# Kernel optimization log

Measured on AMD Instinct MI355X. Metric: run time of the kernel, lower is better.

## Reference

```python
import jax, jax.numpy as jnp
import numpy as np

B, NN, HL = 64, 64, 50
IN_DIM, POS_DIM, ATT_DIM = 384, 64, 256
NEWS_DIM = IN_DIM + POS_DIM  # 448


def setup_inputs() -> dict:
    key = jax.random.key(0)
    ks = jax.random.split(key, 8)
    pos_emb = jax.random.uniform(ks[3], (100, POS_DIM), jnp.float32, -0.1, 0.1)
    pos_emb = pos_emb.at[0].set(0.0)  # initialize() zeros row 0
    return {
        "log_vec": jax.random.normal(ks[0], (B, HL, IN_DIM), jnp.float32),
        "log_mask": jax.random.randint(ks[1], (B, HL), 0, 2, jnp.int32),
        "news_vec": jax.random.normal(ks[2], (B, NN, IN_DIM), jnp.float32),
        "pos_emb": pos_emb,
        "W1": jax.random.normal(ks[4], (ATT_DIM, 2 * NEWS_DIM), jnp.float32) * 0.02,
        "b1": jnp.zeros((ATT_DIM,), jnp.float32),
        "W2": jax.random.normal(ks[5], (1, ATT_DIM), jnp.float32) * 0.02,
        "b2": jnp.zeros((1,), jnp.float32),
    }


def reference(log_vec, log_mask, news_vec, pos_emb, W1, b1, W2, b2):
    b, nn_ = news_vec.shape[:2]
    hl = log_mask.shape[1]
    # append position embeddings (row 0 for candidates, rows 1..hl for history)
    nf = jnp.concatenate(
        [news_vec, jnp.broadcast_to(pos_emb[0], (b, nn_, POS_DIM))], axis=-1)   # (B,NN,ND)
    lf = jnp.concatenate(
        [log_vec, jnp.broadcast_to(pos_emb[1:hl + 1], (b, hl, POS_DIM))], axis=-1)  # (B,HL,ND)
    # affine1(cat[news, log]) == news @ Wn^T + log @ Wl^T + b1 (avoids concat)
    Wn, Wl = W1[:, :NEWS_DIM], W1[:, NEWS_DIM:]
    pn = jnp.einsum('bnd,ad->bna', nf, Wn)   # (B,NN,A)
    pl = jnp.einsum('bhd,ad->bha', lf, Wl)   # (B,HL,A)
    h = jnp.tanh(pn[:, :, None, :] + pl[:, None, :, :] + b1)  # (B,NN,HL,A)
    logits = jnp.einsum('bnha,a->bnh', h, W2[0]) + b2[0]      # (B,NN,HL)
    logits = jnp.where(log_mask[:, None, :] == 0, jnp.float32(-1e9), logits)
    attn = jax.nn.softmax(logits, axis=2)
    user_log_vecs = jnp.einsum('bnh,bhd->bnd', attn, lf)      # (B,NN,ND)
    return user_log_vecs, nf
```

## Files before the change

kernel.cpp:

```cpp
#include <hip/hip_runtime.h>
#include <math.h>

typedef unsigned short u16;
typedef unsigned int   u32;

#define B_       64
#define NN_      64
#define HL_      50
#define IN_DIM   384
#define POS_DIM  64
#define ATT_DIM  256
#define NEWS_DIM 448

typedef __attribute__((ext_vector_type(8))) short short8;
typedef __attribute__((ext_vector_type(4))) float f32x4;

#if __has_builtin(__builtin_amdgcn_exp2f)
#define EXP2F(x) __builtin_amdgcn_exp2f(x)
#else
#define EXP2F(x) exp2f(x)
#endif
#if __has_builtin(__builtin_amdgcn_rcpf)
#define RCPF(x) __builtin_amdgcn_rcpf(x)
#else
#define RCPF(x) (1.0f/(x))
#endif

__device__ __forceinline__ u16 f2bf(float f) {
    union { float f; u32 i; } v; v.f = f;
    u32 r = v.i + 0x7fffu + ((v.i >> 16) & 1u);
    return (u16)(r >> 16);
}
__device__ __forceinline__ float bf2f(u16 u) {
    union { u32 i; float f; } v; v.i = ((u32)u) << 16; return v.f;
}
__device__ __forceinline__ uint2 pack4(float4 v) {
    return make_uint2((u32)f2bf(v.x) | ((u32)f2bf(v.y) << 16),
                      (u32)f2bf(v.z) | ((u32)f2bf(v.w) << 16));
}
__device__ __forceinline__ float fast_tanh(float x) {
    float e = EXP2F(x * 2.88539008f);
    return 1.0f - 2.0f * RCPF(1.0f + e);
}

__global__ __launch_bounds__(256) void prep_k(
    const float* __restrict__ W1, const float* __restrict__ newsv,
    const float* __restrict__ logv, const float* __restrict__ pos,
    u16* __restrict__ Wbf, u16* __restrict__ nv_bf, u16* __restrict__ lf_bf,
    float* __restrict__ nf)
{
    u32 bid = blockIdx.x, tid = threadIdx.x;
    if (bid < 2936u) {
        u32 x = bid & 7u, j = bid >> 3;
        if (j < 192u) {
            u32 idx = j * 256u + tid;
            u32 r = 512u * x + idx / 96u, d4 = idx % 96u;
            float4 v = *(const float4*)(newsv + (size_t)r * IN_DIM + d4 * 4u);
            *(uint2*)(nv_bf + (size_t)r * IN_DIM + d4 * 4u) = pack4(v);
            *(float4*)(nf + (size_t)r * NEWS_DIM + d4 * 4u) = v;
        } else if (j < 342u) {
            u32 idx = (j - 192u) * 256u + tid;
            u32 r = 400u * x + idx / 96u, d4 = idx % 96u;
            float4 v = *(const float4*)(logv + (size_t)r * IN_DIM + d4 * 4u);
            *(uint2*)(lf_bf + (size_t)r * NEWS_DIM + d4 * 4u) = pack4(v);
        } else {
            u32 idx = (j - 342u) * 256u + tid;
            u32 r = 400u * x + idx / 16u, d4 = idx % 16u;
            u32 h = r % HL_;
            float4 v = *(const float4*)(pos + (size_t)(1u + h) * POS_DIM + d4 * 4u);
            *(uint2*)(lf_bf + (size_t)r * NEWS_DIM + IN_DIM + d4 * 4u) = pack4(v);
        }
        return;
    }
    bid -= 2936u;
    if (bid < 224u) {
        u32 i = bid * 256u + tid;
        float4 v = *(const float4*)(W1 + (size_t)i * 4u);
        *(uint2*)(Wbf + (size_t)i * 4u) = pack4(v);
        return;
    }
    bid -= 224u;
    {
        u32 i = bid * 256u + tid;
        u32 r = i / 16u, d4 = i % 16u;
        *(float4*)(nf + (size_t)r * NEWS_DIM + IN_DIM + d4 * 4u) =
            make_float4(0.f, 0.f, 0.f, 0.f);
    }
}

__global__ __launch_bounds__(64) void gemm_k(
    const u16* __restrict__ nv_bf, const u16* __restrict__ lf_bf,
    const u16* __restrict__ Wbf, const float* __restrict__ b1,
    float* __restrict__ pn, float* __restrict__ plT)
{
    int bid = blockIdx.x;
    int lane = threadIdx.x;
    int m = lane & 15, q = lane >> 4;
    int x = bid & 7, j = bid >> 3;
    bool is_pn = j < 128;
    int r0, c0, lda, koff, klen;
    const u16* A;
    if (is_pn) {
        int b = x * 8 + (j >> 4);
        r0 = b * 64 + ((j >> 2) & 3) * 16;
        c0 = (j & 3) * 64;
        A = nv_bf; lda = IN_DIM;   koff = 0;        klen = IN_DIM;
    } else {
        int j2 = j - 128;
        r0 = 400 * x + (j2 >> 2) * 16;
        c0 = (j2 & 3) * 64;
        A = lf_bf; lda = NEWS_DIM; koff = NEWS_DIM; klen = NEWS_DIM;
    }

    f32x4 acc[4];
#pragma unroll
    for (int b = 0; b < 4; b++) acc[b] = (f32x4){0.f, 0.f, 0.f, 0.f};

    const u16* Ap = A + (size_t)(r0 + m) * lda + q * 8;
    const u16* Wp = Wbf + (size_t)(c0 + m) * (2 * NEWS_DIM) + koff + q * 8;

    for (int k = 0; k < klen; k += 32) {
        short8 af, wf[4];
        af = *(const short8*)(Ap + k);
#pragma unroll
        for (int ct = 0; ct < 4; ct++) wf[ct] = *(const short8*)(Wp + ct * 16 * (2 * NEWS_DIM) + k);
#pragma unroll
        for (int ct = 0; ct < 4; ct++)
            acc[ct] = __builtin_amdgcn_mfma_f32_16x16x32_bf16(af, wf[ct], acc[ct], 0, 0, 0);
    }
#pragma unroll
    for (int ct = 0; ct < 4; ct++)
#pragma unroll
        for (int i = 0; i < 4; i++) {
            int gr = r0 + q * 4 + i;
            int gc = c0 + ct * 16 + m;
            float v = acc[ct][i];
            if (is_pn) {
                pn[(size_t)gr * ATT_DIM + gc] = v + b1[gc];
            } else {
                int bb = gr / HL_, hh = gr - bb * HL_;
                plT[(size_t)(bb * ATT_DIM + gc) * HL_ + hh] = v;
            }
        }
}

__global__ __launch_bounds__(256) void attn_out_k(
    const float* __restrict__ pn, const float* __restrict__ plT,
    const float* __restrict__ w2, const int* __restrict__ lmask,
    const u16* __restrict__ lf_bf, float* __restrict__ out)
{
    __shared__ float at_s[4][64];
    int lane = threadIdx.x & 63;
    int wid = __builtin_amdgcn_readfirstlane((int)(threadIdx.x >> 6));
    int x     = blockIdx.x & 7;
    int local = blockIdx.x >> 3;
    int b     = x * 8 + (local >> 4);
    int sub   = local & 15;
    int g     = b * 64 + sub * 4 + wid;
    int n_hl  = (lane < HL_) ? lane : (HL_ - 1);
    const float* pr = pn + (size_t)g * ATT_DIM;
    const float* pl = plT + (size_t)b * ATT_DIM * HL_ + n_hl;

    float a0 = 0.f, a1 = 0.f, a2 = 0.f, a3 = 0.f;
#pragma unroll 4
    for (int a = 0; a < ATT_DIM; a += 4) {
        float4 w4 = *(const float4*)(w2 + a);
        float4 p  = *(const float4*)(pr + a);
        float l0 = pl[(a + 0) * HL_];
        float l1 = pl[(a + 1) * HL_];
        float l2 = pl[(a + 2) * HL_];
        float l3 = pl[(a + 3) * HL_];
        a0 = __builtin_fmaf(fast_tanh(p.x + l0), w4.x, a0);
        a1 = __builtin_fmaf(fast_tanh(p.y + l1), w4.y, a1);
        a2 = __builtin_fmaf(fast_tanh(p.z + l2), w4.z, a2);
        a3 = __builtin_fmaf(fast_tanh(p.w + l3), w4.w, a3);
    }
    float acc = (a0 + a1) + (a2 + a3);
    int mv = (lane < HL_) ? lmask[b * HL_ + lane] : 0;
    float logit = mv ? acc : -1e9f;
    float mx = logit;
#pragma unroll
    for (int o = 32; o > 0; o >>= 1) mx = fmaxf(mx, __shfl_xor(mx, o));
    float e = EXP2F((logit - mx) * 1.44269504f);
    float s = e;
#pragma unroll
    for (int o = 32; o > 0; o >>= 1) s += __shfl_xor(s, o);
    at_s[wid][lane] = e * RCPF(s);

    const u32* lfb32 = (const u32*)(lf_bf + (size_t)b * HL_ * NEWS_DIM);
    int tidx = 192 + (lane & 31);
    float p0 = 0.f, p1 = 0.f, p2 = 0.f, p3 = 0.f,
          p4 = 0.f, p5 = 0.f, p6 = 0.f, p7 = 0.f;
    for (int h = 0; h < HL_; h++) {
        float av = at_s[wid][h];
        const u32* r32 = lfb32 + h * (NEWS_DIM / 2);
        u32 v0 = r32[lane];
        u32 v1 = r32[lane + 64];
        u32 v2 = r32[lane + 128];
        u32 v3 = r32[tidx];
        p0 = fmaf(av, bf2f((u16)v0),         p0);
        p1 = fmaf(av, bf2f((u16)(v0 >> 16)), p1);
        p2 = fmaf(av, bf2f((u16)v1),         p2);
        p3 = fmaf(av, bf2f((u16)(v1 >> 16)), p3);
        p4 = fmaf(av, bf2f((u16)v2),         p4);
        p5 = fmaf(av, bf2f((u16)(v2 >> 16)), p5);
        p6 = fmaf(av, bf2f((u16)v3),         p6);
        p7 = fmaf(av, bf2f((u16)(v3 >> 16)), p7);
    }
    float* orow = out + (size_t)g * NEWS_DIM;
    *(float2*)(orow +       2 * lane) = make_float2(p0, p1);
    *(float2*)(orow + 128 + 2 * lane) = make_float2(p2, p3);
    *(float2*)(orow + 256 + 2 * lane) = make_float2(p4, p5);
    if (lane < 32)
        *(float2*)(orow + 384 + 2 * lane) = make_float2(p6, p7);
}

extern "C" void kernel_launch(void* const* d_in, const int* in_sizes, int n_in,
                              void* d_out, int out_size, void* d_ws, size_t ws_size,
                              hipStream_t stream) {
    const float* logv  = (const float*)d_in[0];
    const int*   lmask = (const int*)d_in[1];
    const float* newsv = (const float*)d_in[2];
    const float* pos   = (const float*)d_in[3];
    const float* W1    = (const float*)d_in[4];
    const float* b1    = (const float*)d_in[5];
    const float* w2    = (const float*)d_in[6];

    float* out = (float*)d_out;
    float* nf  = out + (size_t)B_ * NN_ * NEWS_DIM;

    char* ws = (char*)d_ws;
    u16*   lf_bf = (u16*)(ws + 0);
    u16*   Wbf   = (u16*)(ws + 2867200);
    u16*   nv_bf = (u16*)(ws + 3325952);
    float* pn    = (float*)(ws + 6471680);
    float* plT   = (float*)(ws + 10665984);

    prep_k    <<<3416, 256, 0, stream>>>(W1, newsv, logv, pos,
                                         Wbf, nv_bf, lf_bf, nf);
    gemm_k    <<<1824, 64, 0, stream>>>(nv_bf, lf_bf, Wbf, b1, pn, plT);
    attn_out_k<<<1024, 256, 0, stream>>>(pn, plT, w2, lmask, lf_bf, out);
}
```

Baseline: 127.7 us.

## Split attention reduction across wave pairs to double parallelism in attn_out_k

Each output row is now handled by two waves. Each wave computes half of the ATT_DIM tanh reduction, and the partial logits are combined through shared memory with a barrier. Each wave also produces half of the weighted-sum output columns. The grid doubles and launch bounds request higher occupancy. Softmax is computed redundantly in both waves, and the added barrier may introduce stalls.

```diff
diff --git a/kernel.cpp b/kernel.cpp
--- a/kernel.cpp
+++ b/kernel.cpp
@@ -144,27 +144,32 @@
         }
 }
 
-__global__ __launch_bounds__(256) void attn_out_k(
+__global__ __launch_bounds__(256, 8) void attn_out_k(
     const float* __restrict__ pn, const float* __restrict__ plT,
     const float* __restrict__ w2, const int* __restrict__ lmask,
     const u16* __restrict__ lf_bf, float* __restrict__ out)
 {
+    __shared__ float part[4][64];
     __shared__ float at_s[4][64];
     int lane = threadIdx.x & 63;
     int wid = __builtin_amdgcn_readfirstlane((int)(threadIdx.x >> 6));
+    int pair = wid >> 1;
+    int half = wid & 1;
     int x     = blockIdx.x & 7;
     int local = blockIdx.x >> 3;
-    int b     = x * 8 + (local >> 4);
-    int sub   = local & 15;
-    int g     = b * 64 + sub * 4 + wid;
+    int b     = x * 8 + (local >> 5);
+    int sub   = local & 31;
+    int g     = b * 64 + sub * 2 + pair;
     int n_hl  = (lane < HL_) ? lane : (HL_ - 1);
-    const float* pr = pn + (size_t)g * ATT_DIM;
-    const float* pl = plT + (size_t)b * ATT_DIM * HL_ + n_hl;
+    int aoff  = half * 128;
+    const float* pr  = pn + (size_t)g * ATT_DIM + aoff;
+    const float* pl  = plT + ((size_t)b * ATT_DIM + aoff) * HL_ + n_hl;
+    const float* w2o = w2 + aoff;
 
     float a0 = 0.f, a1 = 0.f, a2 = 0.f, a3 = 0.f;
-#pragma unroll 4
-    for (int a = 0; a < ATT_DIM; a += 4) {
-        float4 w4 = *(const float4*)(w2 + a);
+#pragma unroll 2
+    for (int a = 0; a < 128; a += 4) {
+        float4 w4 = *(const float4*)(w2o + a);
         float4 p  = *(const float4*)(pr + a);
         float l0 = pl[(a + 0) * HL_];
         float l1 = pl[(a + 1) * HL_];
@@ -176,6 +181,10 @@
         a3 = __builtin_fmaf(fast_tanh(p.w + l3), w4.w, a3);
     }
     float acc = (a0 + a1) + (a2 + a3);
+    part[wid][lane] = acc;
+    __syncthreads();
+    acc += part[wid ^ 1][lane];
+
     int mv = (lane < HL_) ? lmask[b * HL_ + lane] : 0;
     float logit = mv ? acc : -1e9f;
     float mx = logit;
@@ -188,31 +197,23 @@
     at_s[wid][lane] = e * RCPF(s);
 
     const u32* lfb32 = (const u32*)(lf_bf + (size_t)b * HL_ * NEWS_DIM);
-    int tidx = 192 + (lane & 31);
-    float p0 = 0.f, p1 = 0.f, p2 = 0.f, p3 = 0.f,
-          p4 = 0.f, p5 = 0.f, p6 = 0.f, p7 = 0.f;
+    int i0 = half ? (lane + 128) : lane;
+    int i1 = half ? (192 + (lane & 31)) : (lane + 64);
+    float p0 = 0.f, p1 = 0.f, p2 = 0.f, p3 = 0.f;
     for (int h = 0; h < HL_; h++) {
         float av = at_s[wid][h];
         const u32* r32 = lfb32 + h * (NEWS_DIM / 2);
-        u32 v0 = r32[lane];
-        u32 v1 = r32[lane + 64];
-        u32 v2 = r32[lane + 128];
-        u32 v3 = r32[tidx];
+        u32 v0 = r32[i0];
+        u32 v1 = r32[i1];
         p0 = fmaf(av, bf2f((u16)v0),         p0);
         p1 = fmaf(av, bf2f((u16)(v0 >> 16)), p1);
         p2 = fmaf(av, bf2f((u16)v1),         p2);
         p3 = fmaf(av, bf2f((u16)(v1 >> 16)), p3);
-        p4 = fmaf(av, bf2f((u16)v2),         p4);
-        p5 = fmaf(av, bf2f((u16)(v2 >> 16)), p5);
-        p6 = fmaf(av, bf2f((u16)v3),         p6);
-        p7 = fmaf(av, bf2f((u16)(v3 >> 16)), p7);
     }
     float* orow = out + (size_t)g * NEWS_DIM;
-    *(float2*)(orow +       2 * lane) = make_float2(p0, p1);
-    *(float2*)(orow + 128 + 2 * lane) = make_float2(p2, p3);
-    *(float2*)(orow + 256 + 2 * lane) = make_float2(p4, p5);
-    if (lane < 32)
-        *(float2*)(orow + 384 + 2 * lane) = make_float2(p6, p7);
+    *(float2*)(orow + 2 * i0) = make_float2(p0, p1);
+    if (half == 0 || lane < 32)
+        *(float2*)(orow + 2 * i1) = make_float2(p2, p3);
 }
 
 extern "C" void kernel_launch(void* const* d_in, const int* in_sizes, int n_in,
@@ -239,5 +240,5 @@
     prep_k    <<<3416, 256, 0, stream>>>(W1, newsv, logv, pos,
                                          Wbf, nv_bf, lf_bf, nf);
     gemm_k    <<<1824, 64, 0, stream>>>(nv_bf, lf_bf, Wbf, b1, pn, plT);
-    attn_out_k<<<1024, 256, 0, stream>>>(pn, plT, w2, lmask, lf_bf, out);
-}
+    attn_out_k<<<2048, 256, 0, stream>>>(pn, plT, w2, lmask, lf_bf, out);
+}
```

Result: no change. 129.0 us (+1.0%).

## Fuse prep, GEMM and attention into one cooperative kernel with grid syncs

Applied to the files above, without the earlier changes.

Merges the three kernel launches into a single cooperative kernel of 1024 blocks that runs the prep phase in a grid-stride loop, then the GEMM phase (four 64-lane GEMM tiles per 256-thread block), then the attention/output phase, with grid-wide syncs between phases. The goal is to remove per-launch overhead and the gaps between kernels. In exchange it adds two grid barriers, only 456 of the 1024 blocks do GEMM work, and a cooperative launch needs all 1024 blocks resident at once.

```diff
diff --git a/kernel.cpp b/kernel.cpp
--- a/kernel.cpp
+++ b/kernel.cpp
@@ -1,5 +1,8 @@
 #include <hip/hip_runtime.h>
+#include <hip/hip_cooperative_groups.h>
 #include <math.h>
+
+namespace cg = cooperative_groups;
 
 typedef unsigned short u16;
 typedef unsigned int   u32;
@@ -43,13 +46,13 @@
     return 1.0f - 2.0f * RCPF(1.0f + e);
 }
 
-__global__ __launch_bounds__(256) void prep_k(
+__device__ __forceinline__ void prep_body(
+    u32 bid, u32 tid,
     const float* __restrict__ W1, const float* __restrict__ newsv,
     const float* __restrict__ logv, const float* __restrict__ pos,
     u16* __restrict__ Wbf, u16* __restrict__ nv_bf, u16* __restrict__ lf_bf,
     float* __restrict__ nf)
 {
-    u32 bid = blockIdx.x, tid = threadIdx.x;
     if (bid < 2936u) {
         u32 x = bid & 7u, j = bid >> 3;
         if (j < 192u) {
@@ -88,131 +91,142 @@
     }
 }
 
-__global__ __launch_bounds__(64) void gemm_k(
-    const u16* __restrict__ nv_bf, const u16* __restrict__ lf_bf,
-    const u16* __restrict__ Wbf, const float* __restrict__ b1,
-    float* __restrict__ pn, float* __restrict__ plT)
-{
-    int bid = blockIdx.x;
-    int lane = threadIdx.x;
-    int m = lane & 15, q = lane >> 4;
-    int x = bid & 7, j = bid >> 3;
-    bool is_pn = j < 128;
-    int r0, c0, lda, koff, klen;
-    const u16* A;
-    if (is_pn) {
-        int b = x * 8 + (j >> 4);
-        r0 = b * 64 + ((j >> 2) & 3) * 16;
-        c0 = (j & 3) * 64;
-        A = nv_bf; lda = IN_DIM;   koff = 0;        klen = IN_DIM;
-    } else {
-        int j2 = j - 128;
-        r0 = 400 * x + (j2 >> 2) * 16;
-        c0 = (j2 & 3) * 64;
-        A = lf_bf; lda = NEWS_DIM; koff = NEWS_DIM; klen = NEWS_DIM;
-    }
-
-    f32x4 acc[4];
-#pragma unroll
-    for (int b = 0; b < 4; b++) acc[b] = (f32x4){0.f, 0.f, 0.f, 0.f};
-
-    const u16* Ap = A + (size_t)(r0 + m) * lda + q * 8;
-    const u16* Wp = Wbf + (size_t)(c0 + m) * (2 * NEWS_DIM) + koff + q * 8;
-
-    for (int k = 0; k < klen; k += 32) {
-        short8 af, wf[4];
-        af = *(const short8*)(Ap + k);
-#pragma unroll
-        for (int ct = 0; ct < 4; ct++) wf[ct] = *(const short8*)(Wp + ct * 16 * (2 * NEWS_DIM) + k);
-#pragma unroll
-        for (int ct = 0; ct < 4; ct++)
-            acc[ct] = __builtin_amdgcn_mfma_f32_16x16x32_bf16(af, wf[ct], acc[ct], 0, 0, 0);
-    }
-#pragma unroll
-    for (int ct = 0; ct < 4; ct++)
-#pragma unroll
-        for (int i = 0; i < 4; i++) {
-            int gr = r0 + q * 4 + i;
-            int gc = c0 + ct * 16 + m;
-            float v = acc[ct][i];
-            if (is_pn) {
-                pn[(size_t)gr * ATT_DIM + gc] = v + b1[gc];
-            } else {
-                int bb = gr / HL_, hh = gr - bb * HL_;
-                plT[(size_t)(bb * ATT_DIM + gc) * HL_ + hh] = v;
-            }
-        }
-}
-
-__global__ __launch_bounds__(256) void attn_out_k(
-    const float* __restrict__ pn, const float* __restrict__ plT,
-    const float* __restrict__ w2, const int* __restrict__ lmask,
-    const u16* __restrict__ lf_bf, float* __restrict__ out)
+__global__ __launch_bounds__(256, 4) void fused_k(
+    const float* __restrict__ W1, const float* __restrict__ newsv,
+    const float* __restrict__ logv, const float* __restrict__ pos,
+    const int* __restrict__ lmask, const float* __restrict__ w2,
+    const float* __restrict__ b1,
+    u16* __restrict__ Wbf, u16* __restrict__ nv_bf, u16* __restrict__ lf_bf,
+    float* __restrict__ nf, float* __restrict__ pn, float* __restrict__ plT,
+    float* __restrict__ out)
 {
     __shared__ float at_s[4][64];
-    int lane = threadIdx.x & 63;
-    int wid = __builtin_amdgcn_readfirstlane((int)(threadIdx.x >> 6));
-    int x     = blockIdx.x & 7;
-    int local = blockIdx.x >> 3;
-    int b     = x * 8 + (local >> 4);
-    int sub   = local & 15;
-    int g     = b * 64 + sub * 4 + wid;
-    int n_hl  = (lane < HL_) ? lane : (HL_ - 1);
-    const float* pr = pn + (size_t)g * ATT_DIM;
-    const float* pl = plT + (size_t)b * ATT_DIM * HL_ + n_hl;
-
-    float a0 = 0.f, a1 = 0.f, a2 = 0.f, a3 = 0.f;
+    u32 bid = blockIdx.x;
+    u32 tid = threadIdx.x;
+    int lane = (int)(tid & 63u);
+    int wid  = __builtin_amdgcn_readfirstlane((int)(tid >> 6));
+
+    for (u32 vb = bid; vb < 3416u; vb += 1024u)
+        prep_body(vb, tid, W1, newsv, logv, pos, Wbf, nv_bf, lf_bf, nf);
+
+    cg::this_grid().sync();
+
+    if (bid < 456u) {
+        int x = (int)(bid & 7u), j = (int)((bid >> 3) * 4u) + wid;
+        int m = lane & 15, q = lane >> 4;
+        bool is_pn = j < 128;
+        int r0, c0, lda, koff, klen;
+        const u16* A;
+        if (is_pn) {
+            int b = x * 8 + (j >> 4);
+            r0 = b * 64 + ((j >> 2) & 3) * 16;
+            c0 = (j & 3) * 64;
+            A = nv_bf; lda = IN_DIM;   koff = 0;        klen = IN_DIM;
+        } else {
+            int j2 = j - 128;
+            r0 = 400 * x + (j2 >> 2) * 16;
+            c0 = (j2 & 3) * 64;
+            A = lf_bf; lda = NEWS_DIM; koff = NEWS_DIM; klen = NEWS_DIM;
+        }
+
+        f32x4 acc[4];
+#pragma unroll
+        for (int b = 0; b < 4; b++) acc[b] = (f32x4){0.f, 0.f, 0.f, 0.f};
+
+        const u16* Ap = A + (size_t)(r0 + m) * lda + q * 8;
+        const u16* Wp = Wbf + (size_t)(c0 + m) * (2 * NEWS_DIM) + koff + q * 8;
+
+        for (int k = 0; k < klen; k += 32) {
+            short8 af, wf[4];
+            af = *(const short8*)(Ap + k);
+#pragma unroll
+            for (int ct = 0; ct < 4; ct++)
+                wf[ct] = *(const short8*)(Wp + ct * 16 * (2 * NEWS_DIM) + k);
+#pragma unroll
+            for (int ct = 0; ct < 4; ct++)
+                acc[ct] = __builtin_amdgcn_mfma_f32_16x16x32_bf16(af, wf[ct], acc[ct], 0, 0, 0);
+        }
+#pragma unroll
+        for (int ct = 0; ct < 4; ct++)
+#pragma unroll
+            for (int i = 0; i < 4; i++) {
+                int gr = r0 + q * 4 + i;
+                int gc = c0 + ct * 16 + m;
+                float v = acc[ct][i];
+                if (is_pn) {
+                    pn[(size_t)gr * ATT_DIM + gc] = v + b1[gc];
+                } else {
+                    int bb = gr / HL_, hh = gr - bb * HL_;
+                    plT[(size_t)(bb * ATT_DIM + gc) * HL_ + hh] = v;
+                }
+            }
+    }
+
+    cg::this_grid().sync();
+
+    {
+        int x     = (int)(bid & 7u);
+        int local = (int)(bid >> 3);
+        int b     = x * 8 + (local >> 4);
+        int sub   = local & 15;
+        int g     = b * 64 + sub * 4 + wid;
+        int n_hl  = (lane < HL_) ? lane : (HL_ - 1);
+        const float* pr = pn + (size_t)g * ATT_DIM;
+        const float* pl = plT + (size_t)b * ATT_DIM * HL_ + n_hl;
+
+        float a0 = 0.f, a1 = 0.f, a2 = 0.f, a3 = 0.f;
 #pragma unroll 4
-    for (int a = 0; a < ATT_DIM; a += 4) {
-        float4 w4 = *(const float4*)(w2 + a);
-        float4 p  = *(const float4*)(pr + a);
-        float l0 = pl[(a + 0) * HL_];
-        float l1 = pl[(a + 1) * HL_];
-        float l2 = pl[(a + 2) * HL_];
-        float l3 = pl[(a + 3) * HL_];
-        a0 = __builtin_fmaf(fast_tanh(p.x + l0), w4.x, a0);
-        a1 = __builtin_fmaf(fast_tanh(p.y + l1), w4.y, a1);
-        a2 = __builtin_fmaf(fast_tanh(p.z + l2), w4.z, a2);
-        a3 = __builtin_fmaf(fast_tanh(p.w + l3), w4.w, a3);
-    }
-    float acc = (a0 + a1) + (a2 + a3);
-    int mv = (lane < HL_) ? lmask[b * HL_ + lane] : 0;
-    float logit = mv ? acc : -1e9f;
-    float mx = logit;
-#pragma unroll
-    for (int o = 32; o > 0; o >>= 1) mx = fmaxf(mx, __shfl_xor(mx, o));
-    float e = EXP2F((logit - mx) * 1.44269504f);
-    float s = e;
-#pragma unroll
-    for (int o = 32; o > 0; o >>= 1) s += __shfl_xor(s, o);
-    at_s[wid][lane] = e * RCPF(s);
-
-    const u32* lfb32 = (const u32*)(lf_bf + (size_t)b * HL_ * NEWS_DIM);
-    int tidx = 192 + (lane & 31);
-    float p0 = 0.f, p1 = 0.f, p2 = 0.f, p3 = 0.f,
-          p4 = 0.f, p5 = 0.f, p6 = 0.f, p7 = 0.f;
-    for (int h = 0; h < HL_; h++) {
-        float av = at_s[wid][h];
-        const u32* r32 = lfb32 + h * (NEWS_DIM / 2);
-        u32 v0 = r32[lane];
-        u32 v1 = r32[lane + 64];
-        u32 v2 = r32[lane + 128];
-        u32 v3 = r32[tidx];
-        p0 = fmaf(av, bf2f((u16)v0),         p0);
-        p1 = fmaf(av, bf2f((u16)(v0 >> 16)), p1);
-        p2 = fmaf(av, bf2f((u16)v1),         p2);
-        p3 = fmaf(av, bf2f((u16)(v1 >> 16)), p3);
-        p4 = fmaf(av, bf2f((u16)v2),         p4);
-        p5 = fmaf(av, bf2f((u16)(v2 >> 16)), p5);
-        p6 = fmaf(av, bf2f((u16)v3),         p6);
-        p7 = fmaf(av, bf2f((u16)(v3 >> 16)), p7);
-    }
-    float* orow = out + (size_t)g * NEWS_DIM;
-    *(float2*)(orow +       2 * lane) = make_float2(p0, p1);
-    *(float2*)(orow + 128 + 2 * lane) = make_float2(p2, p3);
-    *(float2*)(orow + 256 + 2 * lane) = make_float2(p4, p5);
-    if (lane < 32)
-        *(float2*)(orow + 384 + 2 * lane) = make_float2(p6, p7);
+        for (int a = 0; a < ATT_DIM; a += 4) {
+            float4 w4 = *(const float4*)(w2 + a);
+            float4 p  = *(const float4*)(pr + a);
+            float l0 = pl[(a + 0) * HL_];
+            float l1 = pl[(a + 1) * HL_];
+            float l2 = pl[(a + 2) * HL_];
+            float l3 = pl[(a + 3) * HL_];
+            a0 = __builtin_fmaf(fast_tanh(p.x + l0), w4.x, a0);
+            a1 = __builtin_fmaf(fast_tanh(p.y + l1), w4.y, a1);
+            a2 = __builtin_fmaf(fast_tanh(p.z + l2), w4.z, a2);
+            a3 = __builtin_fmaf(fast_tanh(p.w + l3), w4.w, a3);
+        }
+        float acc = (a0 + a1) + (a2 + a3);
+        int mv = (lane < HL_) ? lmask[b * HL_ + lane] : 0;
+        float logit = mv ? acc : -1e9f;
+        float mx = logit;
+#pragma unroll
+        for (int o = 32; o > 0; o >>= 1) mx = fmaxf(mx, __shfl_xor(mx, o));
+        float e = EXP2F((logit - mx) * 1.44269504f);
+        float s = e;
+#pragma unroll
+        for (int o = 32; o > 0; o >>= 1) s += __shfl_xor(s, o);
+        at_s[wid][lane] = e * RCPF(s);
+
+        const u32* lfb32 = (const u32*)(lf_bf + (size_t)b * HL_ * NEWS_DIM);
+        int tidx = 192 + (lane & 31);
+        float p0 = 0.f, p1 = 0.f, p2 = 0.f, p3 = 0.f,
+              p4 = 0.f, p5 = 0.f, p6 = 0.f, p7 = 0.f;
+        for (int h = 0; h < HL_; h++) {
+            float av = at_s[wid][h];
+            const u32* r32 = lfb32 + h * (NEWS_DIM / 2);
+            u32 v0 = r32[lane];
+            u32 v1 = r32[lane + 64];
+            u32 v2 = r32[lane + 128];
+            u32 v3 = r32[tidx];
+            p0 = fmaf(av, bf2f((u16)v0),         p0);
+            p1 = fmaf(av, bf2f((u16)(v0 >> 16)), p1);
+            p2 = fmaf(av, bf2f((u16)v1),         p2);
+            p3 = fmaf(av, bf2f((u16)(v1 >> 16)), p3);
+            p4 = fmaf(av, bf2f((u16)v2),         p4);
+            p5 = fmaf(av, bf2f((u16)(v2 >> 16)), p5);
+            p6 = fmaf(av, bf2f((u16)v3),         p6);
+            p7 = fmaf(av, bf2f((u16)(v3 >> 16)), p7);
+        }
+        float* orow = out + (size_t)g * NEWS_DIM;
+        *(float2*)(orow +       2 * lane) = make_float2(p0, p1);
+        *(float2*)(orow + 128 + 2 * lane) = make_float2(p2, p3);
+        *(float2*)(orow + 256 + 2 * lane) = make_float2(p4, p5);
+        if (lane < 32)
+            *(float2*)(orow + 384 + 2 * lane) = make_float2(p6, p7);
+    }
 }
 
 extern "C" void kernel_launch(void* const* d_in, const int* in_sizes, int n_in,
@@ -236,8 +250,12 @@
     float* pn    = (float*)(ws + 6471680);
     float* plT   = (float*)(ws + 10665984);
 
-    prep_k    <<<3416, 256, 0, stream>>>(W1, newsv, logv, pos,
-                                         Wbf, nv_bf, lf_bf, nf);
-    gemm_k    <<<1824, 64, 0, stream>>>(nv_bf, lf_bf, Wbf, b1, pn, plT);
-    attn_out_k<<<1024, 256, 0, stream>>>(pn, plT, w2, lmask, lf_bf, out);
-}
+    void* args[] = {
+        (void*)&W1, (void*)&newsv, (void*)&logv, (void*)&pos,
+        (void*)&lmask, (void*)&w2, (void*)&b1,
+        (void*)&Wbf, (void*)&nv_bf, (void*)&lf_bf,
+        (void*)&nf, (void*)&pn, (void*)&plT, (void*)&out
+    };
+    hipLaunchCooperativeKernel((const void*)fused_k, dim3(1024), dim3(256),
+                               args, 0, stream);
+}
```

Measured after the change: 354.5 us. +177.6%, slower.

## Store history projection row-major and vectorize attention and pooling loads

Applied to the files above, without the earlier changes.

The GEMM now writes the history projection in row-major (B*HL, A) layout instead of a transposed (B, A, HL) layout. Each lane in the attention kernel can then read its history row with float4 loads instead of four strided scalar loads. The pooling loop switches from four 32-bit loads per h to two 64-bit loads, and the output stores widen to float4. The trade-off is that each lane now reads a distinct 1KB row, so loads across a wavefront are no longer coalesced and must rely on the caches.

```diff
diff --git a/kernel.cpp b/kernel.cpp
--- a/kernel.cpp
+++ b/kernel.cpp
@@ -91,7 +91,7 @@
 __global__ __launch_bounds__(64) void gemm_k(
     const u16* __restrict__ nv_bf, const u16* __restrict__ lf_bf,
     const u16* __restrict__ Wbf, const float* __restrict__ b1,
-    float* __restrict__ pn, float* __restrict__ plT)
+    float* __restrict__ pn, float* __restrict__ pl2)
 {
     int bid = blockIdx.x;
     int lane = threadIdx.x;
@@ -138,14 +138,13 @@
             if (is_pn) {
                 pn[(size_t)gr * ATT_DIM + gc] = v + b1[gc];
             } else {
-                int bb = gr / HL_, hh = gr - bb * HL_;
-                plT[(size_t)(bb * ATT_DIM + gc) * HL_ + hh] = v;
+                pl2[(size_t)gr * ATT_DIM + gc] = v;
             }
         }
 }
 
 __global__ __launch_bounds__(256) void attn_out_k(
-    const float* __restrict__ pn, const float* __restrict__ plT,
+    const float* __restrict__ pn, const float* __restrict__ pl2,
     const float* __restrict__ w2, const int* __restrict__ lmask,
     const u16* __restrict__ lf_bf, float* __restrict__ out)
 {
@@ -158,22 +157,20 @@
     int sub   = local & 15;
     int g     = b * 64 + sub * 4 + wid;
     int n_hl  = (lane < HL_) ? lane : (HL_ - 1);
-    const float* pr = pn + (size_t)g * ATT_DIM;
-    const float* pl = plT + (size_t)b * ATT_DIM * HL_ + n_hl;
+    const float4* w2v = (const float4*)w2;
+    const float4* prv = (const float4*)(pn + (size_t)g * ATT_DIM);
+    const float4* plv = (const float4*)(pl2 + ((size_t)b * HL_ + n_hl) * ATT_DIM);
 
     float a0 = 0.f, a1 = 0.f, a2 = 0.f, a3 = 0.f;
-#pragma unroll 4
-    for (int a = 0; a < ATT_DIM; a += 4) {
-        float4 w4 = *(const float4*)(w2 + a);
-        float4 p  = *(const float4*)(pr + a);
-        float l0 = pl[(a + 0) * HL_];
-        float l1 = pl[(a + 1) * HL_];
-        float l2 = pl[(a + 2) * HL_];
-        float l3 = pl[(a + 3) * HL_];
-        a0 = __builtin_fmaf(fast_tanh(p.x + l0), w4.x, a0);
-        a1 = __builtin_fmaf(fast_tanh(p.y + l1), w4.y, a1);
-        a2 = __builtin_fmaf(fast_tanh(p.z + l2), w4.z, a2);
-        a3 = __builtin_fmaf(fast_tanh(p.w + l3), w4.w, a3);
+#pragma unroll 8
+    for (int a4 = 0; a4 < ATT_DIM / 4; a4++) {
+        float4 w4 = w2v[a4];
+        float4 p  = prv[a4];
+        float4 l  = plv[a4];
+        a0 = __builtin_fmaf(fast_tanh(p.x + l.x), w4.x, a0);
+        a1 = __builtin_fmaf(fast_tanh(p.y + l.y), w4.y, a1);
+        a2 = __builtin_fmaf(fast_tanh(p.z + l.z), w4.z, a2);
+        a3 = __builtin_fmaf(fast_tanh(p.w + l.w), w4.w, a3);
     }
     float acc = (a0 + a1) + (a2 + a3);
     int mv = (lane < HL_) ? lmask[b * HL_ + lane] : 0;
@@ -187,32 +184,29 @@
     for (int o = 32; o > 0; o >>= 1) s += __shfl_xor(s, o);
     at_s[wid][lane] = e * RCPF(s);
 
-    const u32* lfb32 = (const u32*)(lf_bf + (size_t)b * HL_ * NEWS_DIM);
-    int tidx = 192 + (lane & 31);
-    float p0 = 0.f, p1 = 0.f, p2 = 0.f, p3 = 0.f,
-          p4 = 0.f, p5 = 0.f, p6 = 0.f, p7 = 0.f;
+    const uint2* lfb2 = (const uint2*)(lf_bf + (size_t)b * HL_ * NEWS_DIM);
+    int l48 = (lane < 48) ? lane : (lane - 48);
+    int k1  = 64 + l48;
+    float q0 = 0.f, q1 = 0.f, q2 = 0.f, q3 = 0.f;
+    float r0 = 0.f, r1 = 0.f, r2 = 0.f, r3 = 0.f;
     for (int h = 0; h < HL_; h++) {
         float av = at_s[wid][h];
-        const u32* r32 = lfb32 + h * (NEWS_DIM / 2);
-        u32 v0 = r32[lane];
-        u32 v1 = r32[lane + 64];
-        u32 v2 = r32[lane + 128];
-        u32 v3 = r32[tidx];
-        p0 = fmaf(av, bf2f((u16)v0),         p0);
-        p1 = fmaf(av, bf2f((u16)(v0 >> 16)), p1);
-        p2 = fmaf(av, bf2f((u16)v1),         p2);
-        p3 = fmaf(av, bf2f((u16)(v1 >> 16)), p3);
-        p4 = fmaf(av, bf2f((u16)v2),         p4);
-        p5 = fmaf(av, bf2f((u16)(v2 >> 16)), p5);
-        p6 = fmaf(av, bf2f((u16)v3),         p6);
-        p7 = fmaf(av, bf2f((u16)(v3 >> 16)), p7);
+        const uint2* row = lfb2 + h * (NEWS_DIM / 4);
+        uint2 v0 = row[lane];
+        uint2 v1 = row[k1];
+        q0 = fmaf(av, bf2f((u16)v0.x),         q0);
+        q1 = fmaf(av, bf2f((u16)(v0.x >> 16)), q1);
+        q2 = fmaf(av, bf2f((u16)v0.y),         q2);
+        q3 = fmaf(av, bf2f((u16)(v0.y >> 16)), q3);
+        r0 = fmaf(av, bf2f((u16)v1.x),         r0);
+        r1 = fmaf(av, bf2f((u16)(v1.x >> 16)), r1);
+        r2 = fmaf(av, bf2f((u16)v1.y),         r2);
+        r3 = fmaf(av, bf2f((u16)(v1.y >> 16)), r3);
     }
     float* orow = out + (size_t)g * NEWS_DIM;
-    *(float2*)(orow +       2 * lane) = make_float2(p0, p1);
-    *(float2*)(orow + 128 + 2 * lane) = make_float2(p2, p3);
-    *(float2*)(orow + 256 + 2 * lane) = make_float2(p4, p5);
-    if (lane < 32)
-        *(float2*)(orow + 384 + 2 * lane) = make_float2(p6, p7);
+    *(float4*)(orow + 4 * lane) = make_float4(q0, q1, q2, q3);
+    if (lane < 48)
+        *(float4*)(orow + 4 * k1) = make_float4(r0, r1, r2, r3);
 }
 
 extern "C" void kernel_launch(void* const* d_in, const int* in_sizes, int n_in,
@@ -234,10 +228,10 @@
     u16*   Wbf   = (u16*)(ws + 2867200);
     u16*   nv_bf = (u16*)(ws + 3325952);
     float* pn    = (float*)(ws + 6471680);
-    float* plT   = (float*)(ws + 10665984);
+    float* pl2   = (float*)(ws + 10665984);
 
     prep_k    <<<3416, 256, 0, stream>>>(W1, newsv, logv, pos,
                                          Wbf, nv_bf, lf_bf, nf);
-    gemm_k    <<<1824, 64, 0, stream>>>(nv_bf, lf_bf, Wbf, b1, pn, plT);
-    attn_out_k<<<1024, 256, 0, stream>>>(pn, plT, w2, lmask, lf_bf, out);
-}
+    gemm_k    <<<1824, 64, 0, stream>>>(nv_bf, lf_bf, Wbf, b1, pn, pl2);
+    attn_out_k<<<1024, 256, 0, stream>>>(pn, pl2, w2, lmask, lf_bf, out);
+}
```

Result: slower. 138.0 us (+8.1%).
